# Performance work log

Hardware: AMD Instinct MI355X
Metric: run time of the kernel (lower is better)

## Reference

```python
import jax, jax.numpy as jnp
import numpy as np
from functools import partial

B, T_OUT, T_IN, L, D_IN, D_ATT = 8, 256, 512, 128, 128, 128


def setup_inputs() -> dict:
    key = jax.random.key(0)
    ks = jax.random.split(key, 8)
    s = 0.05  # small init scale for numerical stability
    return {
        "inputs": jax.random.normal(ks[0], (B, T_OUT, D_IN), jnp.float32),
        "attended_inputs": jax.random.normal(ks[1], (B, T_IN, D_ATT), jnp.float32),
        "lstm_kernel": jax.random.normal(ks[2], (D_IN, 4 * L), jnp.float32) * s,
        "lstm_rec_kernel": jax.random.normal(ks[3], (L, 4 * L), jnp.float32) * s,
        "lstm_bias": jnp.zeros((4 * L,), jnp.float32),
        "W1": jax.random.normal(ks[4], (D_ATT, L), jnp.float32) * s,
        "b1": jnp.zeros((L,), jnp.float32),
        "W2": jax.random.normal(ks[5], (L, L), jnp.float32) * s,
        "b2": jnp.zeros((L,), jnp.float32),
        "W3": jax.random.normal(ks[6], (L, 1), jnp.float32) * s,
        "b3": jnp.zeros((1,), jnp.float32),
    }


def _lstm(x, Wk, Wr, b):
    # x: (B, T, D_in). Keras gate order: i, f, c(g), o. Zero initial state.
    Bq = x.shape[0]
    h0 = jnp.zeros((Bq, L), x.dtype)
    c0 = jnp.zeros((Bq, L), x.dtype)
    xz = jnp.einsum('btd,dk->btk', x, Wk) + b  # precompute input projection

    def step(carry, zt):
        h, c = carry
        z = zt + h @ Wr
        i, f, g, o = jnp.split(z, 4, axis=-1)
        c_new = jax.nn.sigmoid(f) * c + jax.nn.sigmoid(i) * jnp.tanh(g)
        h_new = jax.nn.sigmoid(o) * jnp.tanh(c_new)
        return (h_new, c_new), h_new

    (h_T, c_T), hs = jax.lax.scan(step, (h0, c0), jnp.swapaxes(xz, 0, 1))
    return jnp.swapaxes(hs, 0, 1), h_T, c_T  # (B, T, L), (B, L), (B, L)


def reference(inputs, attended_inputs, lstm_kernel, lstm_rec_kernel, lstm_bias,
              W1, b1, W2, b2, W3, b3):
    # setup_attended: keys = dense1(attended_inputs)
    keys = attended_inputs @ W1 + b1  # (B, T_in, L)
    x, h, c = _lstm(inputs, lstm_kernel, lstm_rec_kernel, lstm_bias)  # (B, T_out, L)
    q = x @ W2 + b2  # (B, T_out, L)
    # Bahdanau additive score: tanh(keys[:,None] + q[:,:,None]) . W3 -> (B, T_out, T_in)
    t = jnp.tanh(keys[:, None, :, :] + q[:, :, None, :])  # (B, T_out, T_in, L)
    scores = jnp.einsum('bqkl,l->bqk', t, W3[:, 0]) + b3[0]
    attn = jax.nn.softmax(scores, axis=-1)
    weighted = jnp.einsum('bqk,bkd->bqd', attn, attended_inputs)  # (B, T_out, D_att)
    out = jnp.concatenate([x, weighted], axis=2)  # (B, T_out, L + D_att)
    return out, h, c
```

## Files before the change

### kernel.cpp

```cpp
#include <hip/hip_runtime.h>
#include <hip/hip_bf16.h>

#define XZ_OFF   1048576
#define KEYS_OFF 2097152
#define X_OFF    2621440
#define OUT_H    524288
#define OUT_C    525312

#define LDS_BARRIER() __asm__ __volatile__("s_waitcnt lgkmcnt(0)\n\ts_barrier" ::: "memory")

typedef _Float16 f16x8 __attribute__((ext_vector_type(8)));
typedef float fx4 __attribute__((ext_vector_type(4)));

__device__ __forceinline__ float fast_rcp(float x) { return __builtin_amdgcn_rcpf(x); }
__device__ __forceinline__ float fast_sig(float v) { return fast_rcp(1.f + __expf(-v)); }
__device__ __forceinline__ float fast_tanh(float v) { return 2.f * fast_rcp(1.f + __expf(-2.f * v)) - 1.f; }

__global__ __launch_bounds__(256)
void xz_prologue(const float* __restrict__ inp, const float* __restrict__ Wk,
                 const float* __restrict__ bias, float* __restrict__ ws) {
  _Float16* xz16 = (_Float16*)(ws + XZ_OFF);
  __shared__ float ar[8][128];
  const int tid = threadIdx.x;
  const int row0 = blockIdx.x * 8;
  for (int i = tid; i < 8 * 128; i += 256) ar[i >> 7][i & 127] = inp[row0 * 128 + i];
  __syncthreads();
  float acc[8][2];
  const float bb0 = bias[tid], bb1 = bias[tid + 256];
#pragma unroll
  for (int r = 0; r < 8; ++r) { acc[r][0] = bb0; acc[r][1] = bb1; }
  for (int d = 0; d < 128; d += 4) {
    float w0a = Wk[(d + 0) * 512 + tid], w0b = Wk[(d + 0) * 512 + tid + 256];
    float w1a = Wk[(d + 1) * 512 + tid], w1b = Wk[(d + 1) * 512 + tid + 256];
    float w2a = Wk[(d + 2) * 512 + tid], w2b = Wk[(d + 2) * 512 + tid + 256];
    float w3a = Wk[(d + 3) * 512 + tid], w3b = Wk[(d + 3) * 512 + tid + 256];
#pragma unroll
    for (int r = 0; r < 8; ++r) {
      float4 a4 = *(const float4*)&ar[r][d];
      acc[r][0] += a4.x * w0a + a4.y * w1a + a4.z * w2a + a4.w * w3a;
      acc[r][1] += a4.x * w0b + a4.y * w1b + a4.z * w2b + a4.w * w3b;
    }
  }
  const int u = tid & 127, g0 = tid >> 7;
#pragma unroll
  for (int r = 0; r < 8; ++r) {
    const int row = row0 + r, b = row >> 8, t = row & 255;
    const int base = ((t * 8 + b) * 128 + u) * 4;
    xz16[base + g0]     = (_Float16)acc[r][0];
    xz16[base + g0 + 2] = (_Float16)acc[r][1];
  }
}

__global__ __launch_bounds__(512, 1)
void lstm_scan(const float* __restrict__ Wrf, const float* __restrict__ att,
               const float* __restrict__ W1, const float* __restrict__ b1,
               const float* __restrict__ ws, float* __restrict__ out) {
  __shared__ _Float16 hb[2][552];
  __shared__ float ar[16][128];
  const int tid = threadIdx.x;

  if (blockIdx.x >= 2) {
    float* keys = (float*)ws + KEYS_OFF;
    const int row0 = (blockIdx.x - 2) * 16;
    for (int i = tid; i < 16 * 128; i += 512) ar[i >> 7][i & 127] = att[row0 * 128 + i];
    __syncthreads();
    const int l = tid & 127, r0 = tid >> 7;
    float acc[4];
    const float bl = b1[l];
#pragma unroll
    for (int i = 0; i < 4; ++i) acc[i] = bl;
    for (int d = 0; d < 128; d += 4) {
      float w0 = W1[(d + 0) * 128 + l], w1 = W1[(d + 1) * 128 + l];
      float w2 = W1[(d + 2) * 128 + l], w3 = W1[(d + 3) * 128 + l];
#pragma unroll
      for (int i = 0; i < 4; ++i) {
        float4 a4 = *(const float4*)&ar[r0 + 4 * i][d];
        acc[i] += a4.x * w0 + a4.y * w1 + a4.z * w2 + a4.w * w3;
      }
    }
#pragma unroll
    for (int i = 0; i < 4; ++i) keys[(row0 + r0 + 4 * i) * 128 + l] = acc[i];
    return;
  }

  const _Float16* xz16 = (const _Float16*)(ws + XZ_OFF);
  _Float16* x16 = (_Float16*)((float*)ws + X_OFF);
  const int b_base = blockIdx.x * 4;
  const int w = tid >> 6, lane = tid & 63;
  const int q = lane >> 4, p = lane & 15;
  const int b = p & 3, isel = p >> 2;
  const int u = 16 * w + 4 * isel + q;
  const int bg = b_base + b;

  f16x8 afr[4][4];
#pragma unroll
  for (int i = 0; i < 4; ++i) {
    const int col = (p & 3) * 128 + 16 * w + 4 * i + (p >> 2);
#pragma unroll
    for (int kt = 0; kt < 4; ++kt)
#pragma unroll
      for (int j = 0; j < 8; ++j)
        afr[i][kt][j] = (_Float16)Wrf[(kt * 32 + q * 8 + j) * 512 + col];
  }

  {
    _Float16* hp = &hb[0][0];
    for (int i = tid; i < 2 * 552; i += 512) hp[i] = (_Float16)0.f;
  }
  const fx4 zeroC = {0.f, 0.f, 0.f, 0.f};
  float cst = 0.f, hval = 0.f;
  const _Float16* xp = xz16 + (bg * 128 + u) * 4;
  uint2 pf0 = *(const uint2*)(xp);
  uint2 pf1 = *(const uint2*)(xp + 4096);
  uint2 pf2 = *(const uint2*)(xp + 8192);
  __syncthreads();

  const int brow = (p & 3) * 136;
  for (int t = 0; t < 256; ++t) {
    const _Float16* hrow = &hb[t & 1][brow];
    f16x8 bfr[4];
#pragma unroll
    for (int kt = 0; kt < 4; ++kt)
      bfr[kt] = *(const f16x8*)&hrow[kt * 32 + q * 8];
    fx4 acc[4];
#pragma unroll
    for (int i = 0; i < 4; ++i)
      acc[i] = __builtin_amdgcn_mfma_f32_16x16x32_f16(afr[i][0], bfr[0], zeroC, 0, 0, 0);
#pragma unroll
    for (int kt = 1; kt < 4; ++kt)
#pragma unroll
      for (int i = 0; i < 4; ++i)
        acc[i] = __builtin_amdgcn_mfma_f32_16x16x32_f16(afr[i][kt], bfr[kt], acc[i], 0, 0, 0);

    float z[4];
#pragma unroll
    for (int r = 0; r < 4; ++r) {
      float s01 = (isel & 1) ? acc[1][r] : acc[0][r];
      float s23 = (isel & 1) ? acc[3][r] : acc[2][r];
      z[r] = (isel & 2) ? s23 : s01;
    }

    uint2 cur = pf0;
    pf0 = pf1; pf1 = pf2;
    const int t3 = (t + 3 < 256) ? t + 3 : 255;
    pf2 = *(const uint2*)(xp + t3 * 4096);

    const _Float16* cf = (const _Float16*)&cur;
    const float zi = z[0] + (float)cf[0];
    const float zf = z[1] + (float)cf[1];
    const float zg = z[2] + (float)cf[2];
    const float zo = z[3] + (float)cf[3];
    cst = fast_sig(zf) * cst + fast_sig(zi) * fast_tanh(zg);
    hval = fast_sig(zo) * fast_tanh(cst);
    hb[(t + 1) & 1][b * 136 + u] = (_Float16)hval;
    x16[(bg * 256 + t) * 128 + u] = (_Float16)hval;
    LDS_BARRIER();
  }
  out[OUT_H + bg * 128 + u] = hval;
  out[OUT_C + bg * 128 + u] = cst;
}

__global__ __launch_bounds__(256)
void attn_out_k(const float* __restrict__ att, const float* __restrict__ W2c,
                const float* __restrict__ b2c, const float* __restrict__ W3c,
                const float* __restrict__ b3c, const float* __restrict__ ws,
                float* __restrict__ out) {
  const float* keys = ws + KEYS_OFF;
  const _Float16* x16 = (const _Float16*)(ws + X_OFF);
  __shared__ float qp[4][128];
  __shared__ float xr[4][128];
  __shared__ float sc[4][512];
  __shared__ float kt[64][129];
  __shared__ float w3s[128];
  const int tid = threadIdx.x;
  const int b = blockIdx.x >> 6, q0 = (blockIdx.x & 63) * 4;
  const int l = tid & 127, r0 = tid >> 7;
  if (tid < 128) w3s[tid] = W3c[tid];
  for (int i = tid; i < 4 * 128; i += 256)
    xr[i >> 7][i & 127] = (float)x16[(b * 256 + q0) * 128 + i];
  __syncthreads();
  {
    float qa[2];
    const float bl = b2c[l];
    qa[0] = bl; qa[1] = bl;
    for (int d = 0; d < 128; d += 4) {
      float w0 = W2c[(d + 0) * 128 + l], w1 = W2c[(d + 1) * 128 + l];
      float w2v = W2c[(d + 2) * 128 + l], w3v = W2c[(d + 3) * 128 + l];
#pragma unroll
      for (int i = 0; i < 2; ++i) {
        float4 a4 = *(const float4*)&xr[r0 + 2 * i][d];
        qa[i] += a4.x * w0 + a4.y * w1 + a4.z * w2v + a4.w * w3v;
      }
    }
#pragma unroll
    for (int i = 0; i < 2; ++i) {
      int rr = r0 + 2 * i;
      qp[rr][l] = qa[i];
      out[(b * 256 + q0 + rr) * 256 + l] = xr[rr][l];
    }
  }
  const float b3v = b3c[0];
  for (int kt0 = 0; kt0 < 512; kt0 += 64) {
    __syncthreads();
    for (int i = tid; i < 64 * 128; i += 256)
      kt[i >> 7][i & 127] = keys[(b * 512 + kt0 + (i >> 7)) * 128 + (i & 127)];
    __syncthreads();
    {
      const int rr = tid >> 6, k = tid & 63;
      float acc = 0.f;
      for (int ll = 0; ll < 128; ll += 4) {
        float4 q4 = *(const float4*)&qp[rr][ll];
        float4 w4 = *(const float4*)&w3s[ll];
        acc += fast_tanh(kt[k][ll + 0] + q4.x) * w4.x
             + fast_tanh(kt[k][ll + 1] + q4.y) * w4.y
             + fast_tanh(kt[k][ll + 2] + q4.z) * w4.z
             + fast_tanh(kt[k][ll + 3] + q4.w) * w4.w;
      }
      sc[rr][kt0 + k] = acc + b3v;
    }
  }
  __syncthreads();
  {
    const int wave = tid >> 6, lane = tid & 63;
    float v[8];
#pragma unroll
    for (int i = 0; i < 8; ++i) v[i] = sc[wave][lane + i * 64];
    float m = v[0];
#pragma unroll
    for (int i = 1; i < 8; ++i) m = fmaxf(m, v[i]);
#pragma unroll
    for (int off = 32; off > 0; off >>= 1) m = fmaxf(m, __shfl_xor(m, off));
    float e[8], s = 0.f;
#pragma unroll
    for (int i = 0; i < 8; ++i) { e[i] = __expf(v[i] - m); s += e[i]; }
#pragma unroll
    for (int off = 32; off > 0; off >>= 1) s += __shfl_xor(s, off);
    const float inv = fast_rcp(s);
#pragma unroll
    for (int i = 0; i < 8; ++i) sc[wave][lane + i * 64] = e[i] * inv;
  }
  __syncthreads();
  {
    const float* attb = att + b * 512 * 128;
    float wa[2] = {0.f, 0.f};
    for (int k = 0; k < 512; k += 4) {
      float a0 = attb[(k + 0) * 128 + l];
      float a1 = attb[(k + 1) * 128 + l];
      float a2 = attb[(k + 2) * 128 + l];
      float a3 = attb[(k + 3) * 128 + l];
#pragma unroll
      for (int i = 0; i < 2; ++i) {
        float4 p4 = *(const float4*)&sc[r0 + 2 * i][k];
        wa[i] += p4.x * a0 + p4.y * a1 + p4.z * a2 + p4.w * a3;
      }
    }
#pragma unroll
    for (int i = 0; i < 2; ++i)
      out[(b * 256 + q0 + r0 + 2 * i) * 256 + 128 + l] = wa[i];
  }
}

extern "C" void kernel_launch(void* const* d_in, const int* in_sizes, int n_in,
                              void* d_out, int out_size, void* d_ws, size_t ws_size,
                              hipStream_t stream) {
  const float* inputs   = (const float*)d_in[0];
  const float* attended = (const float*)d_in[1];
  const float* Wk       = (const float*)d_in[2];
  const float* Wr       = (const float*)d_in[3];
  const float* bias     = (const float*)d_in[4];
  const float* W1       = (const float*)d_in[5];
  const float* b1       = (const float*)d_in[6];
  const float* W2       = (const float*)d_in[7];
  const float* b2       = (const float*)d_in[8];
  const float* W3       = (const float*)d_in[9];
  const float* b3       = (const float*)d_in[10];
  float* out = (float*)d_out;
  float* ws = (float*)d_ws;

  hipLaunchKernelGGL(xz_prologue, dim3(256), dim3(256), 0, stream, inputs, Wk, bias, ws);
  hipLaunchKernelGGL(lstm_scan, dim3(258), dim3(512), 0, stream,
                     Wr, attended, W1, b1, ws, out);
  hipLaunchKernelGGL(attn_out_k, dim3(512), dim3(256), 0, stream,
                     attended, W2, b2, W3, b3, ws, out);
}
```

Before: 308.5 us.

## Fuse LSTM scan with attention via progress flags so attention overlaps the recurrence

Keys projection moves into the prologue kernel and is stored transposed. The scan and attention kernels merge into one launch. Attention blocks spin on per-batch-group progress counters, which the scan blocks publish every 8 timesteps, and read the fp32 hidden states through atomic loads. This lets attention work overlap the serial recurrence and removes a launch. It relies on all scan blocks being resident alongside the spinning blocks, which risks deadlock if the scheduler doesn't co-schedule them, and it adds an extra full barrier every 8 steps.

```diff
diff --git a/kernel.cpp b/kernel.cpp
--- a/kernel.cpp
+++ b/kernel.cpp
@@ -1,9 +1,10 @@
 #include <hip/hip_runtime.h>
 #include <hip/hip_bf16.h>
 
+#define XF_OFF   0
+#define PROG_OFF 524288
 #define XZ_OFF   1048576
 #define KEYS_OFF 2097152
-#define X_OFF    2621440
 #define OUT_H    524288
 #define OUT_C    525312
 
@@ -17,74 +18,172 @@
 __device__ __forceinline__ float fast_tanh(float v) { return 2.f * fast_rcp(1.f + __expf(-2.f * v)) - 1.f; }
 
 __global__ __launch_bounds__(256)
-void xz_prologue(const float* __restrict__ inp, const float* __restrict__ Wk,
-                 const float* __restrict__ bias, float* __restrict__ ws) {
-  _Float16* xz16 = (_Float16*)(ws + XZ_OFF);
+void prologue_k(const float* __restrict__ inp, const float* __restrict__ Wk,
+                const float* __restrict__ bias, const float* __restrict__ att,
+                const float* __restrict__ W1, const float* __restrict__ b1,
+                float* __restrict__ ws) {
   __shared__ float ar[8][128];
+  __shared__ float ar2[16][128];
   const int tid = threadIdx.x;
-  const int row0 = blockIdx.x * 8;
-  for (int i = tid; i < 8 * 128; i += 256) ar[i >> 7][i & 127] = inp[row0 * 128 + i];
+
+  if (blockIdx.x < 256) {
+    _Float16* xz16 = (_Float16*)(ws + XZ_OFF);
+    const int row0 = blockIdx.x * 8;
+    for (int i = tid; i < 8 * 128; i += 256) ar[i >> 7][i & 127] = inp[row0 * 128 + i];
+    __syncthreads();
+    float acc[8][2];
+    const float bb0 = bias[tid], bb1 = bias[tid + 256];
+#pragma unroll
+    for (int r = 0; r < 8; ++r) { acc[r][0] = bb0; acc[r][1] = bb1; }
+    for (int d = 0; d < 128; d += 4) {
+      float w0a = Wk[(d + 0) * 512 + tid], w0b = Wk[(d + 0) * 512 + tid + 256];
+      float w1a = Wk[(d + 1) * 512 + tid], w1b = Wk[(d + 1) * 512 + tid + 256];
+      float w2a = Wk[(d + 2) * 512 + tid], w2b = Wk[(d + 2) * 512 + tid + 256];
+      float w3a = Wk[(d + 3) * 512 + tid], w3b = Wk[(d + 3) * 512 + tid + 256];
+#pragma unroll
+      for (int r = 0; r < 8; ++r) {
+        float4 a4 = *(const float4*)&ar[r][d];
+        acc[r][0] += a4.x * w0a + a4.y * w1a + a4.z * w2a + a4.w * w3a;
+        acc[r][1] += a4.x * w0b + a4.y * w1b + a4.z * w2b + a4.w * w3b;
+      }
+    }
+    const int u = tid & 127, g0 = tid >> 7;
+#pragma unroll
+    for (int r = 0; r < 8; ++r) {
+      const int row = row0 + r, b = row >> 8, t = row & 255;
+      const int base = ((t * 8 + b) * 128 + u) * 4;
+      xz16[base + g0]     = (_Float16)acc[r][0];
+      xz16[base + g0 + 2] = (_Float16)acc[r][1];
+    }
+    return;
+  }
+
+  if (blockIdx.x == 256 && tid < 2) ((int*)(ws + PROG_OFF))[tid] = 0;
+  const int kb = blockIdx.x - 256;
+  const int row0 = kb * 16;
+  const int bq = row0 >> 9, k0 = row0 & 511;
+  for (int i = tid; i < 16 * 128; i += 256) ar2[i >> 7][i & 127] = att[row0 * 128 + i];
   __syncthreads();
-  float acc[8][2];
-  const float bb0 = bias[tid], bb1 = bias[tid + 256];
-#pragma unroll
-  for (int r = 0; r < 8; ++r) { acc[r][0] = bb0; acc[r][1] = bb1; }
+  const int l = tid & 127, r0 = tid >> 7;
+  float acc[8];
+  const float bl = b1[l];
+#pragma unroll
+  for (int i = 0; i < 8; ++i) acc[i] = bl;
   for (int d = 0; d < 128; d += 4) {
-    float w0a = Wk[(d + 0) * 512 + tid], w0b = Wk[(d + 0) * 512 + tid + 256];
-    float w1a = Wk[(d + 1) * 512 + tid], w1b = Wk[(d + 1) * 512 + tid + 256];
-    float w2a = Wk[(d + 2) * 512 + tid], w2b = Wk[(d + 2) * 512 + tid + 256];
-    float w3a = Wk[(d + 3) * 512 + tid], w3b = Wk[(d + 3) * 512 + tid + 256];
-#pragma unroll
-    for (int r = 0; r < 8; ++r) {
-      float4 a4 = *(const float4*)&ar[r][d];
-      acc[r][0] += a4.x * w0a + a4.y * w1a + a4.z * w2a + a4.w * w3a;
-      acc[r][1] += a4.x * w0b + a4.y * w1b + a4.z * w2b + a4.w * w3b;
-    }
-  }
-  const int u = tid & 127, g0 = tid >> 7;
-#pragma unroll
-  for (int r = 0; r < 8; ++r) {
-    const int row = row0 + r, b = row >> 8, t = row & 255;
-    const int base = ((t * 8 + b) * 128 + u) * 4;
-    xz16[base + g0]     = (_Float16)acc[r][0];
-    xz16[base + g0 + 2] = (_Float16)acc[r][1];
-  }
+    float w0 = W1[(d + 0) * 128 + l], w1 = W1[(d + 1) * 128 + l];
+    float w2 = W1[(d + 2) * 128 + l], w3 = W1[(d + 3) * 128 + l];
+#pragma unroll
+    for (int i = 0; i < 8; ++i) {
+      float4 a4 = *(const float4*)&ar2[r0 * 8 + i][d];
+      acc[i] += a4.x * w0 + a4.y * w1 + a4.z * w2 + a4.w * w3;
+    }
+  }
+  float* kT = ws + KEYS_OFF + (bq * 128 + l) * 512 + k0 + r0 * 8;
+  float4 lo = {acc[0], acc[1], acc[2], acc[3]};
+  float4 hi = {acc[4], acc[5], acc[6], acc[7]};
+  *(float4*)kT = lo;
+  *(float4*)(kT + 4) = hi;
 }
 
-__global__ __launch_bounds__(512, 1)
-void lstm_scan(const float* __restrict__ Wrf, const float* __restrict__ att,
-               const float* __restrict__ W1, const float* __restrict__ b1,
-               const float* __restrict__ ws, float* __restrict__ out) {
-  __shared__ _Float16 hb[2][552];
-  __shared__ float ar[16][128];
+struct ScanS { _Float16 hb[2][576]; };
+struct AttnS {
+  float xr[4][128];
+  float qp[4][128];
+  float sc[4][512];
+  float kc[8][516];
+  float w3s[128];
+};
+
+__global__ __launch_bounds__(512, 6)
+void fused_scan_attn(const float* __restrict__ Wrf, const float* __restrict__ att,
+                     const float* __restrict__ W2c, const float* __restrict__ b2c,
+                     const float* __restrict__ W3c, const float* __restrict__ b3c,
+                     float* __restrict__ ws, float* __restrict__ out) {
+  __shared__ __align__(16) char smem[29312];
   const int tid = threadIdx.x;
+  int* prog = (int*)(ws + PROG_OFF);
+  float* xf = ws + XF_OFF;
 
   if (blockIdx.x >= 2) {
-    float* keys = (float*)ws + KEYS_OFF;
-    const int row0 = (blockIdx.x - 2) * 16;
-    for (int i = tid; i < 16 * 128; i += 512) ar[i >> 7][i & 127] = att[row0 * 128 + i];
-    __syncthreads();
+    AttnS* A = (AttnS*)smem;
+    const int a = blockIdx.x - 2;
+    const int b = a >> 6, q0 = (a & 63) * 4;
     const int l = tid & 127, r0 = tid >> 7;
-    float acc[4];
-    const float bl = b1[l];
-#pragma unroll
-    for (int i = 0; i < 4; ++i) acc[i] = bl;
+    if (tid < 128) A->w3s[tid] = W3c[tid];
+    if (tid == 0) {
+      while (__hip_atomic_load(&prog[b >> 2], __ATOMIC_RELAXED, __HIP_MEMORY_SCOPE_AGENT) < q0 + 4)
+        __builtin_amdgcn_s_sleep(16);
+    }
+    __syncthreads();
+    const int row = b * 256 + q0 + r0;
+    const float xv = __hip_atomic_load(&xf[row * 128 + l], __ATOMIC_RELAXED, __HIP_MEMORY_SCOPE_AGENT);
+    A->xr[r0][l] = xv;
+    out[row * 256 + l] = xv;
+    __syncthreads();
+    float qa = b2c[l];
     for (int d = 0; d < 128; d += 4) {
-      float w0 = W1[(d + 0) * 128 + l], w1 = W1[(d + 1) * 128 + l];
-      float w2 = W1[(d + 2) * 128 + l], w3 = W1[(d + 3) * 128 + l];
-#pragma unroll
-      for (int i = 0; i < 4; ++i) {
-        float4 a4 = *(const float4*)&ar[r0 + 4 * i][d];
-        acc[i] += a4.x * w0 + a4.y * w1 + a4.z * w2 + a4.w * w3;
+      float4 x4 = *(const float4*)&A->xr[r0][d];
+      qa += x4.x * W2c[(d + 0) * 128 + l] + x4.y * W2c[(d + 1) * 128 + l]
+          + x4.z * W2c[(d + 2) * 128 + l] + x4.w * W2c[(d + 3) * 128 + l];
+    }
+    A->qp[r0][l] = qa;
+    const float b3v = b3c[0];
+    float acc0 = b3v, acc1 = b3v, acc2 = b3v, acc3 = b3v;
+    const float* keysT = ws + KEYS_OFF + b * (128 * 512);
+    for (int c = 0; c < 128; c += 8) {
+      __syncthreads();
+      for (int i = tid; i < 8 * 512; i += 512)
+        A->kc[i >> 9][i & 511] = keysT[(c + (i >> 9)) * 512 + (i & 511)];
+      __syncthreads();
+      for (int lp = 0; lp < 8; ++lp) {
+        const float qv = A->qp[r0][c + lp];
+        const float wv = A->w3s[c + lp];
+        acc0 += fast_tanh(A->kc[lp][l]       + qv) * wv;
+        acc1 += fast_tanh(A->kc[lp][l + 128] + qv) * wv;
+        acc2 += fast_tanh(A->kc[lp][l + 256] + qv) * wv;
+        acc3 += fast_tanh(A->kc[lp][l + 384] + qv) * wv;
       }
     }
-#pragma unroll
-    for (int i = 0; i < 4; ++i) keys[(row0 + r0 + 4 * i) * 128 + l] = acc[i];
+    A->sc[r0][l]       = acc0;
+    A->sc[r0][l + 128] = acc1;
+    A->sc[r0][l + 256] = acc2;
+    A->sc[r0][l + 384] = acc3;
+    __syncthreads();
+    {
+      const int wave = tid >> 6, lane = tid & 63;
+      if (wave < 4) {
+        float v[8];
+#pragma unroll
+        for (int i = 0; i < 8; ++i) v[i] = A->sc[wave][lane + i * 64];
+        float m = v[0];
+#pragma unroll
+        for (int i = 1; i < 8; ++i) m = fmaxf(m, v[i]);
+#pragma unroll
+        for (int off = 32; off > 0; off >>= 1) m = fmaxf(m, __shfl_xor(m, off));
+        float e[8], s = 0.f;
+#pragma unroll
+        for (int i = 0; i < 8; ++i) { e[i] = __expf(v[i] - m); s += e[i]; }
+#pragma unroll
+        for (int off = 32; off > 0; off >>= 1) s += __shfl_xor(s, off);
+        const float inv = fast_rcp(s);
+#pragma unroll
+        for (int i = 0; i < 8; ++i) A->sc[wave][lane + i * 64] = e[i] * inv;
+      }
+    }
+    __syncthreads();
+    const float* attb = att + b * (512 * 128);
+    float wa = 0.f;
+    for (int k = 0; k < 512; k += 4) {
+      float4 p4 = *(const float4*)&A->sc[r0][k];
+      wa += p4.x * attb[(k + 0) * 128 + l] + p4.y * attb[(k + 1) * 128 + l]
+          + p4.z * attb[(k + 2) * 128 + l] + p4.w * attb[(k + 3) * 128 + l];
+    }
+    out[row * 256 + 128 + l] = wa;
     return;
   }
 
+  ScanS* S = (ScanS*)smem;
   const _Float16* xz16 = (const _Float16*)(ws + XZ_OFF);
-  _Float16* x16 = (_Float16*)((float*)ws + X_OFF);
   const int b_base = blockIdx.x * 4;
   const int w = tid >> 6, lane = tid & 63;
   const int q = lane >> 4, p = lane & 15;
@@ -102,10 +201,9 @@
       for (int j = 0; j < 8; ++j)
         afr[i][kt][j] = (_Float16)Wrf[(kt * 32 + q * 8 + j) * 512 + col];
   }
-
   {
-    _Float16* hp = &hb[0][0];
-    for (int i = tid; i < 2 * 552; i += 512) hp[i] = (_Float16)0.f;
+    _Float16* hp = &S->hb[0][0];
+    for (int i = tid; i < 2 * 576; i += 512) hp[i] = (_Float16)0.f;
   }
   const fx4 zeroC = {0.f, 0.f, 0.f, 0.f};
   float cst = 0.f, hval = 0.f;
@@ -115,9 +213,9 @@
   uint2 pf2 = *(const uint2*)(xp + 8192);
   __syncthreads();
 
-  const int brow = (p & 3) * 136;
+  const int brow = b * 144;
   for (int t = 0; t < 256; ++t) {
-    const _Float16* hrow = &hb[t & 1][brow];
+    const _Float16* hrow = &S->hb[t & 1][brow];
     f16x8 bfr[4];
 #pragma unroll
     for (int kt = 0; kt < 4; ++kt)
@@ -142,8 +240,6 @@
 
     uint2 cur = pf0;
     pf0 = pf1; pf1 = pf2;
-    const int t3 = (t + 3 < 256) ? t + 3 : 255;
-    pf2 = *(const uint2*)(xp + t3 * 4096);
 
     const _Float16* cf = (const _Float16*)&cur;
     const float zi = z[0] + (float)cf[0];
@@ -152,112 +248,23 @@
     const float zo = z[3] + (float)cf[3];
     cst = fast_sig(zf) * cst + fast_sig(zi) * fast_tanh(zg);
     hval = fast_sig(zo) * fast_tanh(cst);
-    hb[(t + 1) & 1][b * 136 + u] = (_Float16)hval;
-    x16[(bg * 256 + t) * 128 + u] = (_Float16)hval;
-    LDS_BARRIER();
+    S->hb[(t + 1) & 1][brow + u] = (_Float16)hval;
+    __hip_atomic_store(&xf[(bg * 256 + t) * 128 + u], hval,
+                       __ATOMIC_RELAXED, __HIP_MEMORY_SCOPE_AGENT);
+
+    if ((t & 7) == 7) {
+      __syncthreads();
+      if (tid == 0)
+        __hip_atomic_store(&prog[blockIdx.x], t + 1,
+                           __ATOMIC_RELAXED, __HIP_MEMORY_SCOPE_AGENT);
+    } else {
+      LDS_BARRIER();
+    }
+    const int t3 = (t + 3 < 256) ? t + 3 : 255;
+    pf2 = *(const uint2*)(xp + t3 * 4096);
   }
   out[OUT_H + bg * 128 + u] = hval;
   out[OUT_C + bg * 128 + u] = cst;
-}
-
-__global__ __launch_bounds__(256)
-void attn_out_k(const float* __restrict__ att, const float* __restrict__ W2c,
-                const float* __restrict__ b2c, const float* __restrict__ W3c,
-                const float* __restrict__ b3c, const float* __restrict__ ws,
-                float* __restrict__ out) {
-  const float* keys = ws + KEYS_OFF;
-  const _Float16* x16 = (const _Float16*)(ws + X_OFF);
-  __shared__ float qp[4][128];
-  __shared__ float xr[4][128];
-  __shared__ float sc[4][512];
-  __shared__ float kt[64][129];
-  __shared__ float w3s[128];
-  const int tid = threadIdx.x;
-  const int b = blockIdx.x >> 6, q0 = (blockIdx.x & 63) * 4;
-  const int l = tid & 127, r0 = tid >> 7;
-  if (tid < 128) w3s[tid] = W3c[tid];
-  for (int i = tid; i < 4 * 128; i += 256)
-    xr[i >> 7][i & 127] = (float)x16[(b * 256 + q0) * 128 + i];
-  __syncthreads();
-  {
-    float qa[2];
-    const float bl = b2c[l];
-    qa[0] = bl; qa[1] = bl;
-    for (int d = 0; d < 128; d += 4) {
-      float w0 = W2c[(d + 0) * 128 + l], w1 = W2c[(d + 1) * 128 + l];
-      float w2v = W2c[(d + 2) * 128 + l], w3v = W2c[(d + 3) * 128 + l];
-#pragma unroll
-      for (int i = 0; i < 2; ++i) {
-        float4 a4 = *(const float4*)&xr[r0 + 2 * i][d];
-        qa[i] += a4.x * w0 + a4.y * w1 + a4.z * w2v + a4.w * w3v;
-      }
-    }
-#pragma unroll
-    for (int i = 0; i < 2; ++i) {
-      int rr = r0 + 2 * i;
-      qp[rr][l] = qa[i];
-      out[(b * 256 + q0 + rr) * 256 + l] = xr[rr][l];
-    }
-  }
-  const float b3v = b3c[0];
-  for (int kt0 = 0; kt0 < 512; kt0 += 64) {
-    __syncthreads();
-    for (int i = tid; i < 64 * 128; i += 256)
-      kt[i >> 7][i & 127] = keys[(b * 512 + kt0 + (i >> 7)) * 128 + (i & 127)];
-    __syncthreads();
-    {
-      const int rr = tid >> 6, k = tid & 63;
-      float acc = 0.f;
-      for (int ll = 0; ll < 128; ll += 4) {
-        float4 q4 = *(const float4*)&qp[rr][ll];
-        float4 w4 = *(const float4*)&w3s[ll];
-        acc += fast_tanh(kt[k][ll + 0] + q4.x) * w4.x
-             + fast_tanh(kt[k][ll + 1] + q4.y) * w4.y
-             + fast_tanh(kt[k][ll + 2] + q4.z) * w4.z
-             + fast_tanh(kt[k][ll + 3] + q4.w) * w4.w;
-      }
-      sc[rr][kt0 + k] = acc + b3v;
-    }
-  }
-  __syncthreads();
-  {
-    const int wave = tid >> 6, lane = tid & 63;
-    float v[8];
-#pragma unroll
-    for (int i = 0; i < 8; ++i) v[i] = sc[wave][lane + i * 64];
-    float m = v[0];
-#pragma unroll
-    for (int i = 1; i < 8; ++i) m = fmaxf(m, v[i]);
-#pragma unroll
-    for (int off = 32; off > 0; off >>= 1) m = fmaxf(m, __shfl_xor(m, off));
-    float e[8], s = 0.f;
-#pragma unroll
-    for (int i = 0; i < 8; ++i) { e[i] = __expf(v[i] - m); s += e[i]; }
-#pragma unroll
-    for (int off = 32; off > 0; off >>= 1) s += __shfl_xor(s, off);
-    const float inv = fast_rcp(s);
-#pragma unroll
-    for (int i = 0; i < 8; ++i) sc[wave][lane + i * 64] = e[i] * inv;
-  }
-  __syncthreads();
-  {
-    const float* attb = att + b * 512 * 128;
-    float wa[2] = {0.f, 0.f};
-    for (int k = 0; k < 512; k += 4) {
-      float a0 = attb[(k + 0) * 128 + l];
-      float a1 = attb[(k + 1) * 128 + l];
-      float a2 = attb[(k + 2) * 128 + l];
-      float a3 = attb[(k + 3) * 128 + l];
-#pragma unroll
-      for (int i = 0; i < 2; ++i) {
-        float4 p4 = *(const float4*)&sc[r0 + 2 * i][k];
-        wa[i] += p4.x * a0 + p4.y * a1 + p4.z * a2 + p4.w * a3;
-      }
-    }
-#pragma unroll
-    for (int i = 0; i < 2; ++i)
-      out[(b * 256 + q0 + r0 + 2 * i) * 256 + 128 + l] = wa[i];
-  }
 }
 
 extern "C" void kernel_launch(void* const* d_in, const int* in_sizes, int n_in,
@@ -277,9 +284,8 @@
   float* out = (float*)d_out;
   float* ws = (float*)d_ws;
 
-  hipLaunchKernelGGL(xz_prologue, dim3(256), dim3(256), 0, stream, inputs, Wk, bias, ws);
-  hipLaunchKernelGGL(lstm_scan, dim3(258), dim3(512), 0, stream,
-                     Wr, attended, W1, b1, ws, out);
-  hipLaunchKernelGGL(attn_out_k, dim3(512), dim3(256), 0, stream,
-                     attended, W2, b2, W3, b3, ws, out);
+  hipLaunchKernelGGL(prologue_k, dim3(512), dim3(256), 0, stream,
+                     inputs, Wk, bias, attended, W1, b1, ws);
+  hipLaunchKernelGGL(fused_scan_attn, dim3(514), dim3(512), 0, stream,
+                     Wr, attended, W2, b2, W3, b3, ws, out);
 }
```

Result: slower. 677.2 us (+119.5%).
